# Kernel optimization log

Measured on AMD Instinct MI355X. Metric: run time of the kernel, lower is better.

The kernel has to match this reference:

```python
import jax, jax.numpy as jnp
import numpy as np

C = 4          # number of low-frequency rFFT coefficients kept
EPS = 1e-12    # LayerNorm eps


def setup_inputs() -> dict:
    key = jax.random.key(0)
    k1, k2 = jax.random.split(key)
    B, S, H = 16, 2048, 1024
    input_tensor = jax.random.normal(k1, (B, S, H), dtype=jnp.float32)
    sqrt_beta = jax.random.normal(k2, (1, 1, H), dtype=jnp.float32)
    ln_gamma = jnp.ones((H,), dtype=jnp.float32)
    ln_beta = jnp.zeros((H,), dtype=jnp.float32)
    return {
        "input_tensor": input_tensor,
        "sqrt_beta": sqrt_beta,
        "ln_gamma": ln_gamma,
        "ln_beta": ln_beta,
    }


def _layer_norm(x, gamma, beta):
    mean = jnp.mean(x, axis=-1, keepdims=True)
    var = jnp.mean((x - mean) ** 2, axis=-1, keepdims=True)  # biased, like torch
    return (x - mean) * jax.lax.rsqrt(var + EPS) * gamma + beta


def reference(input_tensor, sqrt_beta, ln_gamma, ln_beta):
    B, S, H = input_tensor.shape
    x = jnp.fft.rfft(input_tensor, axis=1, norm="ortho")  # [B, S//2+1, H] complex
    freq = jnp.arange(x.shape[1])[None, :, None]
    low = jnp.where(freq < C, x, 0.0)                      # zero all coeffs >= c
    low_pass = jnp.fft.irfft(low, n=S, axis=1, norm="ortho")
    high_pass = input_tensor - low_pass
    seq_emb_fft = low_pass + (sqrt_beta ** 2) * high_pass
    # Dropout(0.5) treated as identity (eval mode) for a deterministic reference.
    return _layer_norm(seq_emb_fft + input_tensor, ln_gamma, ln_beta)
```

## Files before the change

### kernel.cpp

```cpp
#include <hip/hip_runtime.h>


constexpr int Sc = 2048;
constexpr int Hc = 1024;
constexpr float TWO_PI_OVER_S = 6.283185307179586f / (float)Sc;

typedef float nfloat4 __attribute__((ext_vector_type(4)));

__device__ __forceinline__ void sincos7(int s, float w[7]) {
    float sn1, cs1;
    sincosf(TWO_PI_OVER_S * (float)s, &sn1, &cs1);
    const float cs2 = fmaf(2.f * cs1, cs1, -1.f);
    const float sn2 = 2.f * sn1 * cs1;
    const float cs3 = cs1 * cs2 - sn1 * sn2;
    const float sn3 = sn1 * cs2 + cs1 * sn2;
    w[0] = 1.f; w[1] = cs1; w[2] = sn1; w[3] = cs2; w[4] = sn2; w[5] = cs3; w[6] = sn3;
}

__global__ __launch_bounds__(256) void freq_coeff_partial(
    const float* __restrict__ x, float* __restrict__ coefp,
    int B, int schunk) {
    const int tid   = threadIdx.x;
    const int b     = blockIdx.y;
    const int chunk = blockIdx.x;
    const int s0    = chunk * schunk;

    const float4* __restrict__ xb =
        reinterpret_cast<const float4*>(x) + (size_t)b * Sc * (Hc / 4) + tid;

    float acc[7][4];
#pragma unroll
    for (int j = 0; j < 7; ++j)
#pragma unroll
        for (int e = 0; e < 4; ++e) acc[j][e] = 0.f;

    for (int si = 0; si < schunk; si += 4) {
        float4 v[4];
#pragma unroll
        for (int r = 0; r < 4; ++r)
            v[r] = xb[(size_t)(s0 + si + r) * (Hc / 4)];
#pragma unroll
        for (int r = 0; r < 4; ++r) {
            float w[7];
            sincos7(s0 + si + r, w);
            const float vv[4] = {v[r].x, v[r].y, v[r].z, v[r].w};
#pragma unroll
            for (int j = 0; j < 7; ++j)
#pragma unroll
                for (int e = 0; e < 4; ++e)
                    acc[j][e] = fmaf(w[j], vv[e], acc[j][e]);
        }
    }

    float4* cp = reinterpret_cast<float4*>(coefp) +
                 ((size_t)chunk * B + b) * 7 * (Hc / 4) + tid;
#pragma unroll
    for (int j = 0; j < 7; ++j) {
        float4 o = {acc[j][0], acc[j][1], acc[j][2], acc[j][3]};
        cp[(size_t)j * (Hc / 4)] = o;
    }
}

__global__ __launch_bounds__(256) void coeff_reduce(
    const float* __restrict__ coefp, float* __restrict__ coef,
    int CK, int n4) {
    const int i = blockIdx.x * 256 + threadIdx.x;
    if (i >= n4) return;
    const float4* __restrict__ p = reinterpret_cast<const float4*>(coefp) + i;
    float4 s = {0.f, 0.f, 0.f, 0.f};
    for (int c = 0; c < CK; ++c) {
        const float4 v = p[(size_t)c * n4];
        s.x += v.x; s.y += v.y; s.z += v.z; s.w += v.w;
    }
    reinterpret_cast<float4*>(coef)[i] = s;
}

__global__ __launch_bounds__(256) void freq_ln_kernel(
    const float* __restrict__ x, const float* __restrict__ coef,
    const float* __restrict__ sqb, const float* __restrict__ gamma,
    const float* __restrict__ lbeta, float* __restrict__ out) {
    const int tid = threadIdx.x;
    const int b   = blockIdx.y;
    const int s0  = blockIdx.x * 4;
    const size_t rowBase = ((size_t)b * Sc + s0) * (Hc / 4) + tid;

    const float4 sb4 = reinterpret_cast<const float4*>(sqb)[tid];
    const float4 g4  = reinterpret_cast<const float4*>(gamma)[tid];
    const float4 be4 = reinterpret_cast<const float4*>(lbeta)[tid];
    const float bb[4] = {sb4.x, sb4.y, sb4.z, sb4.w};
    const float gg[4] = {g4.x, g4.y, g4.z, g4.w};
    const float be[4] = {be4.x, be4.y, be4.z, be4.w};
    float ap[4], am[4];
#pragma unroll
    for (int e = 0; e < 4; ++e) {
        const float t = bb[e] * bb[e];
        ap[e] = 1.f + t;
        am[e] = (1.f - t) * (1.f / (float)Sc);
    }

    const float4* __restrict__ CF =
        reinterpret_cast<const float4*>(coef) + (size_t)b * 7 * (Hc / 4) + tid;
    float cf[7][4];
#pragma unroll
    for (int j = 0; j < 7; ++j) {
        const float4 t = CF[(size_t)j * (Hc / 4)];
        cf[j][0] = t.x; cf[j][1] = t.y; cf[j][2] = t.z; cf[j][3] = t.w;
    }

    float4 xv[4];
#pragma unroll
    for (int r = 0; r < 4; ++r)
        xv[r] = reinterpret_cast<const float4*>(x)[rowBase + (size_t)r * (Hc / 4)];

    float y[4][4], s1[4], s2[4];
#pragma unroll
    for (int r = 0; r < 4; ++r) {
        float w[7];
        sincos7(s0 + r, w);
#pragma unroll
        for (int j = 1; j < 7; ++j) w[j] *= 2.f;
        const float xx[4] = {xv[r].x, xv[r].y, xv[r].z, xv[r].w};
        s1[r] = 0.f; s2[r] = 0.f;
#pragma unroll
        for (int e = 0; e < 4; ++e) {
            float lp = cf[0][e];
#pragma unroll
            for (int j = 1; j < 7; ++j) lp = fmaf(cf[j][e], w[j], lp);
            const float yy = fmaf(ap[e], xx[e], am[e] * lp);
            y[r][e] = yy;
            s1[r] += yy;
            s2[r] = fmaf(yy, yy, s2[r]);
        }
    }

    const int lane = tid & 63, wv = tid >> 6;
#pragma unroll
    for (int off = 32; off > 0; off >>= 1) {
#pragma unroll
        for (int r = 0; r < 4; ++r) {
            s1[r] += __shfl_down(s1[r], off, 64);
            s2[r] += __shfl_down(s2[r], off, 64);
        }
    }
    __shared__ float sm[4][8];
    if (lane == 0) {
#pragma unroll
        for (int r = 0; r < 4; ++r) { sm[wv][r] = s1[r]; sm[wv][4 + r] = s2[r]; }
    }
    __syncthreads();

#pragma unroll
    for (int r = 0; r < 4; ++r) {
        const float m  = (sm[0][r] + sm[1][r] + sm[2][r] + sm[3][r]) * (1.f / (float)Hc);
        const float q  = (sm[0][4 + r] + sm[1][4 + r] + sm[2][4 + r] + sm[3][4 + r]) * (1.f / (float)Hc);
        const float inv = rsqrtf(fmaf(-m, m, q) + 1e-12f);
        nfloat4 o;
        o.x = fmaf((y[r][0] - m) * inv, gg[0], be[0]);
        o.y = fmaf((y[r][1] - m) * inv, gg[1], be[1]);
        o.z = fmaf((y[r][2] - m) * inv, gg[2], be[2]);
        o.w = fmaf((y[r][3] - m) * inv, gg[3], be[3]);
        __builtin_nontemporal_store(o, reinterpret_cast<nfloat4*>(out) + rowBase + (size_t)r * (Hc / 4));
    }
}

extern "C" void kernel_launch(void* const* d_in, const int* in_sizes, int n_in,
                              void* d_out, int out_size, void* d_ws, size_t ws_size,
                              hipStream_t stream) {
    const float* x     = (const float*)d_in[0];
    const float* sqb   = (const float*)d_in[1];
    const float* gamma = (const float*)d_in[2];
    const float* lbeta = (const float*)d_in[3];
    float* out = (float*)d_out;

    const int B = in_sizes[0] / (Sc * Hc);
    const size_t coefElems = (size_t)B * 7 * Hc;
    const size_t coefBytes = coefElems * sizeof(float);

    int CK = 64;
    while (CK > 1 && (size_t)(CK + 1) * coefBytes > ws_size) CK >>= 1;

    float* coefp = (float*)d_ws;
    float* coef  = (CK == 1) ? coefp : coefp + CK * coefElems;

    const int schunk = Sc / CK;
    dim3 g1(CK, B);
    freq_coeff_partial<<<g1, 256, 0, stream>>>(x, coefp, B, schunk);

    if (CK > 1) {
        const int n4 = (int)(coefElems / 4);
        coeff_reduce<<<(n4 + 255) / 256, 256, 0, stream>>>(coefp, coef, CK, n4);
    }

    dim3 g2(Sc / 4, B);
    freq_ln_kernel<<<g2, 256, 0, stream>>>(x, coef, sqb, gamma, lbeta, out);
}
```

Before: 276.5 us.

## Double sequence chunks, scalarize coefficient reduce, prescale coefficients, add occupancy hints

Raises the number of sequence chunks in the coefficient pass from 64 to 128, doubling grid parallelism at the cost of more partial-sum traffic in the reduction. The reduce kernel switches to scalar loads with more threads and an unrolled loop. The LayerNorm kernel folds the 2x and am scaling into the coefficients once per thread and issues x loads earlier. Launch bounds now request 8 blocks per CU, which may constrain registers and cause spills.

Result: slower. 343.8 us (+24.3%).

```diff
diff --git a/kernel.cpp b/kernel.cpp
--- a/kernel.cpp
+++ b/kernel.cpp
@@ -3,6 +3,7 @@
 
 constexpr int Sc = 2048;
 constexpr int Hc = 1024;
+constexpr int H4 = Hc / 4;
 constexpr float TWO_PI_OVER_S = 6.283185307179586f / (float)Sc;
 
 typedef float nfloat4 __attribute__((ext_vector_type(4)));
@@ -17,7 +18,7 @@
     w[0] = 1.f; w[1] = cs1; w[2] = sn1; w[3] = cs2; w[4] = sn2; w[5] = cs3; w[6] = sn3;
 }
 
-__global__ __launch_bounds__(256) void freq_coeff_partial(
+__global__ __launch_bounds__(256, 8) void freq_coeff_partial(
     const float* __restrict__ x, float* __restrict__ coefp,
     int B, int schunk) {
     const int tid   = threadIdx.x;
@@ -26,7 +27,7 @@
     const int s0    = chunk * schunk;
 
     const float4* __restrict__ xb =
-        reinterpret_cast<const float4*>(x) + (size_t)b * Sc * (Hc / 4) + tid;
+        reinterpret_cast<const float4*>(x) + (size_t)b * Sc * H4 + tid;
 
     float acc[7][4];
 #pragma unroll
@@ -38,7 +39,7 @@
         float4 v[4];
 #pragma unroll
         for (int r = 0; r < 4; ++r)
-            v[r] = xb[(size_t)(s0 + si + r) * (Hc / 4)];
+            v[r] = xb[(size_t)(s0 + si + r) * H4];
 #pragma unroll
         for (int r = 0; r < 4; ++r) {
             float w[7];
@@ -53,80 +54,82 @@
     }
 
     float4* cp = reinterpret_cast<float4*>(coefp) +
-                 ((size_t)chunk * B + b) * 7 * (Hc / 4) + tid;
+                 ((size_t)chunk * B + b) * 7 * H4 + tid;
 #pragma unroll
     for (int j = 0; j < 7; ++j) {
         float4 o = {acc[j][0], acc[j][1], acc[j][2], acc[j][3]};
-        cp[(size_t)j * (Hc / 4)] = o;
+        cp[(size_t)j * H4] = o;
     }
 }
 
-__global__ __launch_bounds__(256) void coeff_reduce(
+__global__ __launch_bounds__(256, 8) void coeff_reduce(
     const float* __restrict__ coefp, float* __restrict__ coef,
-    int CK, int n4) {
+    int CK, int n) {
     const int i = blockIdx.x * 256 + threadIdx.x;
-    if (i >= n4) return;
-    const float4* __restrict__ p = reinterpret_cast<const float4*>(coefp) + i;
-    float4 s = {0.f, 0.f, 0.f, 0.f};
-    for (int c = 0; c < CK; ++c) {
-        const float4 v = p[(size_t)c * n4];
-        s.x += v.x; s.y += v.y; s.z += v.z; s.w += v.w;
-    }
-    reinterpret_cast<float4*>(coef)[i] = s;
+    if (i >= n) return;
+    const float* __restrict__ p = coefp + i;
+    float s = 0.f;
+#pragma unroll 8
+    for (int c = 0; c < CK; ++c) s += p[(size_t)c * n];
+    coef[i] = s;
 }
 
-__global__ __launch_bounds__(256) void freq_ln_kernel(
+__global__ __launch_bounds__(256, 8) void freq_ln_kernel(
     const float* __restrict__ x, const float* __restrict__ coef,
     const float* __restrict__ sqb, const float* __restrict__ gamma,
     const float* __restrict__ lbeta, float* __restrict__ out) {
     const int tid = threadIdx.x;
     const int b   = blockIdx.y;
     const int s0  = blockIdx.x * 4;
-    const size_t rowBase = ((size_t)b * Sc + s0) * (Hc / 4) + tid;
+    const size_t rowBase = ((size_t)b * Sc + s0) * H4 + tid;
+
+    float4 xv[4];
+#pragma unroll
+    for (int r = 0; r < 4; ++r)
+        xv[r] = reinterpret_cast<const float4*>(x)[rowBase + (size_t)r * H4];
 
     const float4 sb4 = reinterpret_cast<const float4*>(sqb)[tid];
     const float4 g4  = reinterpret_cast<const float4*>(gamma)[tid];
     const float4 be4 = reinterpret_cast<const float4*>(lbeta)[tid];
-    const float bb[4] = {sb4.x, sb4.y, sb4.z, sb4.w};
     const float gg[4] = {g4.x, g4.y, g4.z, g4.w};
     const float be[4] = {be4.x, be4.y, be4.z, be4.w};
     float ap[4], am[4];
+    {
+        const float bb[4] = {sb4.x, sb4.y, sb4.z, sb4.w};
 #pragma unroll
-    for (int e = 0; e < 4; ++e) {
-        const float t = bb[e] * bb[e];
-        ap[e] = 1.f + t;
-        am[e] = (1.f - t) * (1.f / (float)Sc);
+        for (int e = 0; e < 4; ++e) {
+            const float t = bb[e] * bb[e];
+            ap[e] = 1.f + t;
+            am[e] = (1.f - t) * (1.f / (float)Sc);
+        }
     }
 
     const float4* __restrict__ CF =
-        reinterpret_cast<const float4*>(coef) + (size_t)b * 7 * (Hc / 4) + tid;
-    float cf[7][4];
+        reinterpret_cast<const float4*>(coef) + (size_t)b * 7 * H4 + tid;
+    float cfx[7][4];
 #pragma unroll
     for (int j = 0; j < 7; ++j) {
-        const float4 t = CF[(size_t)j * (Hc / 4)];
-        cf[j][0] = t.x; cf[j][1] = t.y; cf[j][2] = t.z; cf[j][3] = t.w;
+        const float4 t = CF[(size_t)j * H4];
+        const float sc = (j == 0) ? 1.f : 2.f;
+        cfx[j][0] = t.x * am[0] * sc;
+        cfx[j][1] = t.y * am[1] * sc;
+        cfx[j][2] = t.z * am[2] * sc;
+        cfx[j][3] = t.w * am[3] * sc;
     }
-
-    float4 xv[4];
-#pragma unroll
-    for (int r = 0; r < 4; ++r)
-        xv[r] = reinterpret_cast<const float4*>(x)[rowBase + (size_t)r * (Hc / 4)];
 
     float y[4][4], s1[4], s2[4];
 #pragma unroll
     for (int r = 0; r < 4; ++r) {
         float w[7];
         sincos7(s0 + r, w);
-#pragma unroll
-        for (int j = 1; j < 7; ++j) w[j] *= 2.f;
         const float xx[4] = {xv[r].x, xv[r].y, xv[r].z, xv[r].w};
         s1[r] = 0.f; s2[r] = 0.f;
 #pragma unroll
         for (int e = 0; e < 4; ++e) {
-            float lp = cf[0][e];
+            float lp = cfx[0][e];
 #pragma unroll
-            for (int j = 1; j < 7; ++j) lp = fmaf(cf[j][e], w[j], lp);
-            const float yy = fmaf(ap[e], xx[e], am[e] * lp);
+            for (int j = 1; j < 7; ++j) lp = fmaf(cfx[j][e], w[j], lp);
+            const float yy = fmaf(ap[e], xx[e], lp);
             y[r][e] = yy;
             s1[r] += yy;
             s2[r] = fmaf(yy, yy, s2[r]);
@@ -159,7 +162,7 @@
         o.y = fmaf((y[r][1] - m) * inv, gg[1], be[1]);
         o.z = fmaf((y[r][2] - m) * inv, gg[2], be[2]);
         o.w = fmaf((y[r][3] - m) * inv, gg[3], be[3]);
-        __builtin_nontemporal_store(o, reinterpret_cast<nfloat4*>(out) + rowBase + (size_t)r * (Hc / 4));
+        __builtin_nontemporal_store(o, reinterpret_cast<nfloat4*>(out) + rowBase + (size_t)r * H4);
     }
 }
 
@@ -176,19 +179,19 @@
     const size_t coefElems = (size_t)B * 7 * Hc;
     const size_t coefBytes = coefElems * sizeof(float);
 
-    int CK = 64;
+    int CK = 128;
     while (CK > 1 && (size_t)(CK + 1) * coefBytes > ws_size) CK >>= 1;
 
     float* coefp = (float*)d_ws;
-    float* coef  = (CK == 1) ? coefp : coefp + CK * coefElems;
+    float* coef  = (CK == 1) ? coefp : coefp + (size_t)CK * coefElems;
 
     const int schunk = Sc / CK;
     dim3 g1(CK, B);
     freq_coeff_partial<<<g1, 256, 0, stream>>>(x, coefp, B, schunk);
 
     if (CK > 1) {
-        const int n4 = (int)(coefElems / 4);
-        coeff_reduce<<<(n4 + 255) / 256, 256, 0, stream>>>(coefp, coef, CK, n4);
+        const int n = (int)coefElems;
+        coeff_reduce<<<(n + 255) / 256, 256, 0, stream>>>(coefp, coef, CK, n);
     }
 
     dim3 g2(Sc / 4, B);
```
